# Kernel tuning notes

Measured on AMD Instinct MI355X. Metric: run time of the kernel, lower is better.

Reference implementation:

```python
import jax, jax.numpy as jnp
import numpy as np

B, D, N, R = 2048, 6, 256, 16


def setup_inputs() -> dict:
    key = jax.random.key(0)
    k_x, k_L, k_q, k_k, k_v, k_o = jax.random.split(key, 6)
    return {
        "x": jax.random.normal(k_x, (B, D, N), dtype=jnp.float32),
        "L": jax.random.normal(k_L, (B, N, N), dtype=jnp.float32),
        "Aq": jax.random.normal(k_q, (R, D), dtype=jnp.float32),
        "Ak": jax.random.normal(k_k, (R, D), dtype=jnp.float32),
        "Av": jax.random.normal(k_v, (R, D), dtype=jnp.float32),
        "Ao": jax.random.normal(k_o, (1, R), dtype=jnp.float32),
    }


def reference(x, L, Aq, Ak, Av, Ao):
    # numNeighbors: count of entries >= 1 in row 0 of each sample's L, plus 1
    numN = jnp.sum((L[:, 0, :] >= 1).astype(jnp.float32), axis=1).reshape(-1, 1, 1) + 1.0  # [B,1,1]
    # Q/K/V projections with tanh: [r,d] x [B,d,N] -> [B,r,N]
    Q = jnp.tanh(jnp.einsum("rd,bdn->brn", Aq, x))
    K = jnp.tanh(jnp.einsum("rd,bdn->brn", Ak, x))
    V = jnp.tanh(jnp.einsum("rd,bdn->brn", Av, x))
    # attention over the small r x r score matrix, scaled by sqrt(neighbor count)
    scores = jnp.einsum("brn,bsn->brs", Q, K) / jnp.sqrt(numN)  # [B,r,r]
    attn = jax.nn.softmax(scores, axis=2)
    o = jnp.einsum("brs,bsn->brn", attn, V)  # [B,r,N]
    H = jax.nn.silu(jnp.einsum("or,brn->bon", Ao, o))[:, 0, :]  # [B,N]
    return (jnp.sum(H, axis=1) ** 2)[:, None]  # [B,1]
```

## Files before the change

kernel.cpp:

```cpp
#include <hip/hip_runtime.h>

namespace {

constexpr int Dd = 6;
constexpr int Nn = 256;
constexpr int Rr = 16;

typedef __attribute__((ext_vector_type(8))) short bf16x8;
typedef __attribute__((ext_vector_type(4))) float f32x4;
typedef __attribute__((ext_vector_type(4))) int i32x4;

__device__ __forceinline__ float fast_tanh(float xv) {
  float e = __builtin_amdgcn_exp2f(xv * 2.8853900817779268f);
  return fmaf(-2.0f, __builtin_amdgcn_rcpf(e + 1.0f), 1.0f);
}

__device__ __forceinline__ unsigned pack_bf16(float a, float b) {
  unsigned r;
  asm("v_cvt_pk_bf16_f32 %0, %1, %2" : "=v"(r) : "v"(a), "v"(b));
  return r;
}

__global__ __launch_bounds__(256) void att_h_fused(
    const float* __restrict__ x,
    const float* __restrict__ L,
    const float* __restrict__ Aq,
    const float* __restrict__ Ak,
    const float* __restrict__ Av,
    const float* __restrict__ Ao,
    float* __restrict__ out,
    int B)
{
  const int tid  = threadIdx.x;
  const int wv   = tid >> 6;
  const int lane = tid & 63;
  const int b    = blockIdx.x * 4 + wv;
  if (b >= B) return;

  const float* xb = x + (size_t)b * (Dd * Nn);

  float xc[Dd][4];
#pragma unroll
  for (int d = 0; d < Dd; ++d) {
    const float4 t = *(const float4*)(xb + d * Nn + lane * 4);
    xc[d][0] = t.x; xc[d][1] = t.y; xc[d][2] = t.z; xc[d][3] = t.w;
  }

  const float4 lr = *(const float4*)(L + (size_t)b * Nn * Nn + lane * 4);
  float cnt = (float)(lr.x >= 1.0f) + (float)(lr.y >= 1.0f) +
              (float)(lr.z >= 1.0f) + (float)(lr.w >= 1.0f);
#pragma unroll
  for (int o = 1; o < 64; o <<= 1) cnt += __shfl_xor(cnt, o);
  const float scale = rsqrtf(cnt + 1.0f);

  const int r     = lane & 15;
  const int quart = lane >> 4;
  float aqr[Dd], akr[Dd];
#pragma unroll
  for (int p = 0; p < 3; ++p) {
    const float2 a = *(const float2*)(Aq + r * Dd + 2 * p);
    const float2 c = *(const float2*)(Ak + r * Dd + 2 * p);
    aqr[2 * p] = a.x; aqr[2 * p + 1] = a.y;
    akr[2 * p] = c.x; akr[2 * p + 1] = c.y;
  }

  f32x4 acc0 = {0.f, 0.f, 0.f, 0.f}, acc1 = {0.f, 0.f, 0.f, 0.f};
#pragma unroll 2
  for (int kb = 0; kb < 8; ++kb) {
    const float* xw = xb + kb * 32 + quart * 8;
    float xa[Dd][8];
#pragma unroll
    for (int d = 0; d < Dd; ++d) {
      const float4 t0 = *(const float4*)(xw + d * Nn);
      const float4 t1 = *(const float4*)(xw + d * Nn + 4);
      xa[d][0] = t0.x; xa[d][1] = t0.y; xa[d][2] = t0.z; xa[d][3] = t0.w;
      xa[d][4] = t1.x; xa[d][5] = t1.y; xa[d][6] = t1.z; xa[d][7] = t1.w;
    }
    float qv[8], kv[8];
#pragma unroll
    for (int j = 0; j < 8; ++j) {
      float aq = 0.0f, ak = 0.0f;
#pragma unroll
      for (int d = 0; d < Dd; ++d) {
        aq = fmaf(aqr[d], xa[d][j], aq);
        ak = fmaf(akr[d], xa[d][j], ak);
      }
      qv[j] = fast_tanh(aq);
      kv[j] = fast_tanh(ak);
    }
    i32x4 qp, kp;
#pragma unroll
    for (int p = 0; p < 4; ++p) {
      qp[p] = (int)pack_bf16(qv[2 * p], qv[2 * p + 1]);
      kp[p] = (int)pack_bf16(kv[2 * p], kv[2 * p + 1]);
    }
    const bf16x8 qa = __builtin_bit_cast(bf16x8, qp);
    const bf16x8 ka = __builtin_bit_cast(bf16x8, kp);
    if (kb & 1)
      acc1 = __builtin_amdgcn_mfma_f32_16x16x32_bf16(qa, ka, acc1, 0, 0, 0);
    else
      acc0 = __builtin_amdgcn_mfma_f32_16x16x32_bf16(qa, ka, acc0, 0, 0, 0);
  }

  const float4 ao4 = *(const float4*)(Ao + quart * 4);
  const float aoarr[4] = {ao4.x, ao4.y, ao4.z, ao4.w};
  float wp = 0.0f;
#pragma unroll
  for (int j = 0; j < 4; ++j) {
    const float sc = (acc0[j] + acc1[j]) * scale;
    float mj = sc;
#pragma unroll
    for (int o = 1; o < 16; o <<= 1) mj = fmaxf(mj, __shfl_xor(mj, o));
    const float ej = __builtin_amdgcn_exp2f((sc - mj) * 1.4426950408889634f);
    float sj = ej;
#pragma unroll
    for (int o = 1; o < 16; o <<= 1) sj += __shfl_xor(sj, o);
    wp = fmaf(aoarr[j], ej * __builtin_amdgcn_rcpf(sj), wp);
  }
  wp += __shfl_xor(wp, 16);
  wp += __shfl_xor(wp, 32);
  float wb[Rr];
#pragma unroll
  for (int s = 0; s < Rr; ++s) wb[s] = __shfl(wp, s);

  float hsum = 0.0f;
#pragma unroll
  for (int c = 0; c < 4; ++c) {
    float h = 0.0f;
#pragma unroll
    for (int s = 0; s < Rr; ++s) {
      float av = 0.0f;
#pragma unroll
      for (int d = 0; d < Dd; ++d) av = fmaf(Av[s * Dd + d], xc[d][c], av);
      h = fmaf(wb[s], fast_tanh(av), h);
    }
    hsum += h * __builtin_amdgcn_rcpf(
                    1.0f + __builtin_amdgcn_exp2f(-1.4426950408889634f * h));
  }
#pragma unroll
  for (int o = 1; o < 64; o <<= 1) hsum += __shfl_xor(hsum, o);
  if (lane == 0) out[b] = hsum * hsum;
}

}

extern "C" void kernel_launch(void* const* d_in, const int* in_sizes, int n_in,
                              void* d_out, int out_size, void* d_ws, size_t ws_size,
                              hipStream_t stream) {
  const float* x  = (const float*)d_in[0];
  const float* L  = (const float*)d_in[1];
  const float* Aq = (const float*)d_in[2];
  const float* Ak = (const float*)d_in[3];
  const float* Av = (const float*)d_in[4];
  const float* Ao = (const float*)d_in[5];
  float* out = (float*)d_out;

  const int B = in_sizes[0] / (Dd * Nn);
  att_h_fused<<<dim3((B + 3) / 4), dim3(256), 0, stream>>>(x, L, Aq, Ak, Av, Ao, out, B);
}
```

Before: 18.33 us.

## Split each sample across two wavefronts with LDS-staged x and reduction

Each block now handles one sample with two wavefronts, each covering half of the N dimension. x is staged once into LDS and reused for both the QK MFMA pass and the V/H pass, so the global re-reads of x go away. Partial score accumulators and H sums are combined through shared memory with two __syncthreads. This doubles the wave count to raise parallelism and shortens per-wave latency, at the cost of block-level sync and the bounds check being dropped (B must be exact).

```diff
diff --git a/kernel.cpp b/kernel.cpp
--- a/kernel.cpp
+++ b/kernel.cpp
@@ -21,29 +21,31 @@
   return r;
 }
 
-__global__ __launch_bounds__(256) void att_h_fused(
+__global__ __launch_bounds__(128, 4) void att_h_fused(
     const float* __restrict__ x,
     const float* __restrict__ L,
     const float* __restrict__ Aq,
     const float* __restrict__ Ak,
     const float* __restrict__ Av,
     const float* __restrict__ Ao,
-    float* __restrict__ out,
-    int B)
+    float* __restrict__ out)
 {
+  __shared__ __align__(16) float xs[2][Dd][128];
+  __shared__ __align__(16) f32x4 accbuf[2][64];
+  __shared__ float hs[2];
+
+  const int b    = blockIdx.x;
   const int tid  = threadIdx.x;
-  const int wv   = tid >> 6;
+  const int h    = tid >> 6;
   const int lane = tid & 63;
-  const int b    = blockIdx.x * 4 + wv;
-  if (b >= B) return;
 
   const float* xb = x + (size_t)b * (Dd * Nn);
 
-  float xc[Dd][4];
 #pragma unroll
-  for (int d = 0; d < Dd; ++d) {
-    const float4 t = *(const float4*)(xb + d * Nn + lane * 4);
-    xc[d][0] = t.x; xc[d][1] = t.y; xc[d][2] = t.z; xc[d][3] = t.w;
+  for (int i = 0; i < 3; ++i) {
+    const int d = 2 * i + (lane >> 5);
+    const int c = (lane & 31) * 4;
+    *(float4*)&xs[h][d][c] = *(const float4*)(xb + d * Nn + h * 128 + c);
   }
 
   const float4 lr = *(const float4*)(L + (size_t)b * Nn * Nn + lane * 4);
@@ -66,13 +68,13 @@
 
   f32x4 acc0 = {0.f, 0.f, 0.f, 0.f}, acc1 = {0.f, 0.f, 0.f, 0.f};
 #pragma unroll 2
-  for (int kb = 0; kb < 8; ++kb) {
-    const float* xw = xb + kb * 32 + quart * 8;
+  for (int kb = 0; kb < 4; ++kb) {
+    const int nw = kb * 32 + quart * 8;
     float xa[Dd][8];
 #pragma unroll
     for (int d = 0; d < Dd; ++d) {
-      const float4 t0 = *(const float4*)(xw + d * Nn);
-      const float4 t1 = *(const float4*)(xw + d * Nn + 4);
+      const float4 t0 = *(const float4*)&xs[h][d][nw];
+      const float4 t1 = *(const float4*)&xs[h][d][nw + 4];
       xa[d][0] = t0.x; xa[d][1] = t0.y; xa[d][2] = t0.z; xa[d][3] = t0.w;
       xa[d][4] = t1.x; xa[d][5] = t1.y; xa[d][6] = t1.z; xa[d][7] = t1.w;
     }
@@ -102,12 +104,17 @@
       acc0 = __builtin_amdgcn_mfma_f32_16x16x32_bf16(qa, ka, acc0, 0, 0, 0);
   }
 
+  accbuf[h][lane] = acc0 + acc1;
+  __syncthreads();
+  const f32x4 other = accbuf[1 - h][lane];
+  const f32x4 acc   = acc0 + acc1 + other;
+
   const float4 ao4 = *(const float4*)(Ao + quart * 4);
   const float aoarr[4] = {ao4.x, ao4.y, ao4.z, ao4.w};
   float wp = 0.0f;
 #pragma unroll
   for (int j = 0; j < 4; ++j) {
-    const float sc = (acc0[j] + acc1[j]) * scale;
+    const float sc = acc[j] * scale;
     float mj = sc;
 #pragma unroll
     for (int o = 1; o < 16; o <<= 1) mj = fmaxf(mj, __shfl_xor(mj, o));
@@ -125,21 +132,29 @@
 
   float hsum = 0.0f;
 #pragma unroll
-  for (int c = 0; c < 4; ++c) {
-    float h = 0.0f;
+  for (int c = 0; c < 2; ++c) {
+    float xcv[Dd];
+#pragma unroll
+    for (int d = 0; d < Dd; ++d) xcv[d] = xs[h][d][lane * 2 + c];
+    float hv = 0.0f;
 #pragma unroll
     for (int s = 0; s < Rr; ++s) {
       float av = 0.0f;
 #pragma unroll
-      for (int d = 0; d < Dd; ++d) av = fmaf(Av[s * Dd + d], xc[d][c], av);
-      h = fmaf(wb[s], fast_tanh(av), h);
+      for (int d = 0; d < Dd; ++d) av = fmaf(Av[s * Dd + d], xcv[d], av);
+      hv = fmaf(wb[s], fast_tanh(av), hv);
     }
-    hsum += h * __builtin_amdgcn_rcpf(
-                    1.0f + __builtin_amdgcn_exp2f(-1.4426950408889634f * h));
+    hsum += hv * __builtin_amdgcn_rcpf(
+                     1.0f + __builtin_amdgcn_exp2f(-1.4426950408889634f * hv));
   }
 #pragma unroll
   for (int o = 1; o < 64; o <<= 1) hsum += __shfl_xor(hsum, o);
-  if (lane == 0) out[b] = hsum * hsum;
+  if (lane == 0) hs[h] = hsum;
+  __syncthreads();
+  if (tid == 0) {
+    const float tot = hs[0] + hs[1];
+    out[b] = tot * tot;
+  }
 }
 
 }
@@ -156,5 +171,5 @@
   float* out = (float*)d_out;
 
   const int B = in_sizes[0] / (Dd * Nn);
-  att_h_fused<<<dim3((B + 3) / 4), dim3(256), 0, stream>>>(x, L, Aq, Ak, Av, Ao, out, B);
+  att_h_fused<<<dim3(B), dim3(128), 0, stream>>>(x, L, Aq, Ak, Av, Ao, out);
 }
```

After: 17.17 us. 6.4% less time.
